# Performance work log

Measured on AMD Instinct MI355X. Metric: run time of the kernel, lower is better.

## Reference

```python
import jax, jax.numpy as jnp
import numpy as np

D = 256          # embed_dim
NH = 4           # num_heads
NE = 16          # num_hyperedges
TC = 512         # text_channels
WIN = 64         # window size
EPS = 1e-5


def setup_inputs() -> dict:
    key = jax.random.key(0)
    ks = jax.random.split(key, 20)
    s = 0.02
    return {
        "feature_map": jax.random.normal(ks[0], (8, 256, 64, 64), jnp.float32),
        "text_features": jax.random.normal(ks[1], (8, 64, TC), jnp.float32),
        # qkv_gen: Conv2d(256->256,1x1), GELU, Conv2d(256->768,3x3,pad1), GroupNorm(4,768)
        "conv1_w": jax.random.normal(ks[2], (D, 256, 1, 1), jnp.float32) * s,
        "conv1_b": jnp.zeros((D,), jnp.float32),
        "conv2_w": jax.random.normal(ks[3], (3 * D, D, 3, 3), jnp.float32) * s,
        "conv2_b": jnp.zeros((3 * D,), jnp.float32),
        "gn_w": jnp.ones((3 * D,), jnp.float32),
        "gn_b": jnp.zeros((3 * D,), jnp.float32),
        # shared nn.MultiheadAttention params
        "in_proj_w": jax.random.normal(ks[4], (3 * D, D), jnp.float32) * s,
        "in_proj_b": jnp.zeros((3 * D,), jnp.float32),
        "out_proj_w": jax.random.normal(ks[5], (D, D), jnp.float32) * s,
        "out_proj_b": jnp.zeros((D,), jnp.float32),
        # text_adapter Linear(512->256)
        "txt_w": jax.random.normal(ks[6], (D, TC), jnp.float32) * s,
        "txt_b": jnp.zeros((D,), jnp.float32),
        # edge_predictor: Linear(512->256), GELU, Linear(256->16)
        "ep1_w": jax.random.normal(ks[7], (D, 2 * D), jnp.float32) * s,
        "ep1_b": jnp.zeros((D,), jnp.float32),
        "ep2_w": jax.random.normal(ks[8], (NE, D), jnp.float32) * s,
        "ep2_b": jnp.zeros((NE,), jnp.float32),
    }


def _gelu(x):
    return jax.nn.gelu(x, approximate=False)  # torch default is exact erf GELU


def _conv(x, w, b, pad):
    y = jax.lax.conv_general_dilated(x, w, (1, 1), [(pad, pad), (pad, pad)],
                                     dimension_numbers=("NCHW", "OIHW", "NCHW"))
    return y + b[None, :, None, None]


def _group_norm(x, w, b, groups=4):
    B, C, H, W = x.shape
    xg = x.reshape(B, groups, C // groups, H, W)
    mu = xg.mean(axis=(2, 3, 4), keepdims=True)
    var = xg.var(axis=(2, 3, 4), keepdims=True)
    xg = (xg - mu) * jax.lax.rsqrt(var + EPS)
    return xg.reshape(B, C, H, W) * w[None, :, None, None] + b[None, :, None, None]


def _mha(q, k, v, in_w, in_b, out_w, out_b):
    # torch nn.MultiheadAttention (batch_first), same-dim q/k/v
    Wq, Wk, Wv = in_w[:D], in_w[D:2 * D], in_w[2 * D:]
    bq, bk, bv = in_b[:D], in_b[D:2 * D], in_b[2 * D:]
    dh = D // NH

    def split(x, W, bias):
        y = x @ W.T + bias                      # [B,L,D]
        Bv, L, _ = y.shape
        return y.reshape(Bv, L, NH, dh).transpose(0, 2, 1, 3)  # [B,H,L,dh]

    qh, kh, vh = split(q, Wq, bq), split(k, Wk, bk), split(v, Wv, bv)
    scores = jnp.einsum("bhqd,bhkd->bhqk", qh, kh) / jnp.sqrt(jnp.float32(dh))
    attn = jax.nn.softmax(scores, axis=-1)
    o = jnp.einsum("bhqk,bhkd->bhqd", attn, vh)
    Bv, _, Lq, _ = o.shape
    o = o.transpose(0, 2, 1, 3).reshape(Bv, Lq, D)
    return o @ out_w.T + out_b


def reference(feature_map, text_features, conv1_w, conv1_b, conv2_w, conv2_b,
              gn_w, gn_b, in_proj_w, in_proj_b, out_proj_w, out_proj_b,
              txt_w, txt_b, ep1_w, ep1_b, ep2_w, ep2_b):
    B, C, H, W = feature_map.shape
    N = H * W
    # qkv_gen
    x = _gelu(_conv(feature_map, conv1_w, conv1_b, 0))
    qkv = _group_norm(_conv(x, conv2_w, conv2_b, 1), gn_w, gn_b)
    q, k, v = jnp.split(qkv, 3, axis=1)                    # each [B,D,H,W]
    to_seq = lambda t: t.reshape(B, D, N).transpose(0, 2, 1)  # [B,N,D]
    q_seq, k_seq, v_seq = to_seq(q), to_seq(k), to_seq(v)

    # text_adapter: Linear then AdaptiveAvgPool1d(4) over sequence (L=64 -> 4 bins of 16)
    t = text_features @ txt_w.T + txt_b                    # [B,L,D]
    L = t.shape[1]
    text_feat = t.reshape(B, 4, L // 4, D).mean(axis=2)    # [B,4,D]

    # hierarchical attention
    nw = N // WIN
    q_win = q_seq.reshape(B * nw, WIN, D)
    k_win = k_seq.reshape(B * nw, WIN, D)
    v_win = v_seq.reshape(B * nw, WIN, D)
    local = _mha(q_win, k_win, v_win, in_proj_w, in_proj_b, out_proj_w, out_proj_b)
    local = local.reshape(B, nw, WIN, D)
    global_q = local.mean(axis=2)                          # [B,nw,D]
    glob = _mha(global_q, text_feat, text_feat, in_proj_w, in_proj_b, out_proj_w, out_proj_b)
    glob = jnp.broadcast_to(glob[:, :, None, :], (B, nw, WIN, D))

    combined = jnp.concatenate([local.reshape(B, N, D), glob.reshape(B, N, D)], axis=-1)
    h = _gelu(combined @ ep1_w.T + ep1_b)
    return jax.nn.sigmoid(h @ ep2_w.T + ep2_b)             # [B,N,16]
```

## Files before the change

kernel.cpp:

```cpp
#include <hip/hip_runtime.h>

#define DEV __device__ __forceinline__

typedef __attribute__((ext_vector_type(8))) short bfx8;
typedef __attribute__((ext_vector_type(4))) float fx4;

typedef __attribute__((address_space(3))) unsigned int as3_u32;
typedef const __attribute__((address_space(1))) unsigned int as1_u32c;

DEV void gl_lds16(const void* g, const void* l) {
  __builtin_amdgcn_global_load_lds((as1_u32c*)(unsigned long long)g,
                                   (as3_u32*)(unsigned long long)l, 16, 0, 0);
}

DEV short f2bf(float f) {
  unsigned u = __float_as_uint(f);
  u += 0x7fffu + ((u >> 16) & 1u);
  return (short)(u >> 16);
}
DEV float bf2f(short s) {
  return __uint_as_float(((unsigned)(unsigned short)s) << 16);
}
DEV float gelu_f(float x) { return 0.5f * x * (1.0f + erff(x * 0.70710678118654752f)); }

#define MFMA16(acc, a, b) (acc) = __builtin_amdgcn_mfma_f32_16x16x32_bf16((a), (b), (acc), 0, 0, 0)

struct CvtSeg { const float* src; short* dst; int n; };
struct CvtArgs { CvtSeg s[7]; };

__global__ __launch_bounds__(256) void cvt_multi(CvtArgs a) {
  CvtSeg s = a.s[blockIdx.y];
  int i = ((int)blockIdx.x * 256 + (int)threadIdx.x) * 8;
  if (i >= s.n) return;
  bfx8 o;
  #pragma unroll
  for (int j = 0; j < 8; ++j) o[j] = f2bf(s.src[i + j]);
  *(bfx8*)(s.dst + i) = o;
}

__global__ __launch_bounds__(256) void cvt_conv2w(const float* src, short* dst) {
  int oc = (int)blockIdx.x * 256 + (int)threadIdx.x;
  const float* s = src + (long)oc * 9;
  float t[9];
  #pragma unroll
  for (int j = 0; j < 9; ++j) t[j] = s[j];
  #pragma unroll
  for (int tap = 0; tap < 9; ++tap)
    dst[(long)tap * (768 * 256) + oc] = f2bf(t[tap]);
}

__global__ __launch_bounds__(256) void transpose_wo(const float* ow, short* WoT) {
  __shared__ float tile[64][65];
  int c0 = blockIdx.x * 64, d0 = blockIdx.y * 64;
  int tp = threadIdx.x & 63, tr = threadIdx.x >> 6;
  #pragma unroll
  for (int i = 0; i < 16; ++i) {
    int c = tr + i * 4;
    tile[c][tp] = ow[(long)(c0 + c) * 256 + d0 + tp];
  }
  __syncthreads();
  #pragma unroll
  for (int i = 0; i < 16; ++i) {
    int d = tr + i * 4;
    WoT[(long)(d0 + d) * 256 + c0 + tp] = f2bf(tile[tp][d]);
  }
}

__global__ __launch_bounds__(64) void ebc2(const float* e1w, const float* e1b, const float* ob, float* ebc) {
  int n = blockIdx.x, lane = threadIdx.x;
  float s = 0.0f;
  #pragma unroll
  for (int i = 0; i < 4; ++i) {
    int c = lane + 64 * i;
    s += ob[c] * e1w[(long)n * 512 + c];
  }
  #pragma unroll
  for (int off = 1; off < 64; off <<= 1) s += __shfl_xor(s, off);
  if (lane == 0) ebc[n] = e1b[n] + s;
}

DEV int axc(int p, int c) { return p * 260 + (c ^ (((p >> 2) & 7) << 2)); }

__global__ __launch_bounds__(256) void tc1(const float* fm, const short* W1bf,
                                           const float* b1, short* xP) {
  __shared__ float Af[64 * 260];
  const int lane = threadIdx.x & 63, wv = threadIdx.x >> 6;
  const int lg = lane >> 4, li = lane & 15;
  const int y = blockIdx.x & 63, b = blockIdx.x >> 6;
  const float* src = fm + (long)b * 256 * 4096 + y * 64;
  #pragma unroll
  for (int i = 0; i < 16; ++i) {
    int chunk = i * 256 + (int)threadIdx.x;
    int c = chunk >> 4;
    int q = chunk & 15;
    fx4 v = *(const fx4*)(src + (long)c * 4096 + q * 4);
    #pragma unroll
    for (int j = 0; j < 4; ++j) Af[axc(q * 4 + j, c)] = v[j];
  }
  __syncthreads();

  fx4 acc[4][4] = {};
  const short* Bb = W1bf + (long)(wv * 64 + li) * 256 + lg * 8;
  for (int c0 = 0; c0 < 256; c0 += 32) {
    bfx8 af[4], bfr[4];
    #pragma unroll
    for (int mi = 0; mi < 4; ++mi) {
      int p = mi * 16 + li;
      fx4 lo = *(const fx4*)(&Af[axc(p, c0 + lg * 8)]);
      fx4 hi = *(const fx4*)(&Af[axc(p, c0 + lg * 8 + 4)]);
      bfx8 t;
      t[0] = f2bf(lo[0]); t[1] = f2bf(lo[1]); t[2] = f2bf(lo[2]); t[3] = f2bf(lo[3]);
      t[4] = f2bf(hi[0]); t[5] = f2bf(hi[1]); t[6] = f2bf(hi[2]); t[7] = f2bf(hi[3]);
      af[mi] = t;
    }
    #pragma unroll
    for (int ni = 0; ni < 4; ++ni) bfr[ni] = *(const bfx8*)(Bb + ni * 16 * 256 + c0);
    #pragma unroll
    for (int mi = 0; mi < 4; ++mi)
      #pragma unroll
      for (int ni = 0; ni < 4; ++ni) MFMA16(acc[mi][ni], af[mi], bfr[ni]);
  }

  short* dstP = xP + ((long)b * 66 * 66 + (long)(y + 1) * 66 + 1) * 256;
  #pragma unroll
  for (int mi = 0; mi < 4; ++mi)
    #pragma unroll
    for (int ni = 0; ni < 4; ++ni) {
      int col = wv * 64 + ni * 16 + li;
      float bias = b1[col];
      #pragma unroll
      for (int r = 0; r < 4; ++r) {
        int x = mi * 16 + 4 * lg + r;
        dstP[(long)x * 256 + col] = f2bf(gelu_f(acc[mi][ni][r] + bias));
      }
    }
}

struct GemmP {
  const short* A; const short* B; void* O;
  const float* biasN; const float* biasM; const float* rowbias;
  long lda, ldb, ldo, sA, sB, sO;
  int M, N, K, outF32, act, padHW;
  int aShift;
  long sBN, sBM;
};

__global__ __launch_bounds__(256) void gemm128(GemmP g) {
  __shared__ short As[128 * 32];
  __shared__ short Bs[128 * 32];
  const int lane = threadIdx.x & 63, wv = threadIdx.x >> 6;
  const int wm = wv >> 1, wn = wv & 1;
  const int lg = lane >> 4, li = lane & 15;
  const int m0 = blockIdx.y * 128, n0 = blockIdx.x * 128, z = blockIdx.z;
  const short* A = g.A + (long)z * g.sA + (long)(n0 >> 8) * g.aShift;
  const short* B = g.B + (long)z * g.sB;
  const int srow = wv * 16 + (lane >> 2);
  const int scol = (lane & 3) * 8;
  const short* pA0 = A + (long)(m0 + srow) * g.lda + scol;
  const short* pA1 = A + (long)(m0 + 64 + srow) * g.lda + scol;
  const short* pB0 = B + (long)(n0 + srow) * g.ldb + scol;
  const short* pB1 = B + (long)(n0 + 64 + srow) * g.ldb + scol;
  short* ldsA = As + wv * 512;
  short* ldsB = Bs + wv * 512;
  const short* aRd = As + (wm * 64 + li) * 32 + lg * 8;
  const short* bRd = Bs + (wn * 64 + li) * 32 + lg * 8;

  fx4 acc[4][4] = {};
  for (int kc = 0; kc < g.K; kc += 32) {
    gl_lds16(pA0 + kc, ldsA);
    gl_lds16(pA1 + kc, ldsA + 2048);
    gl_lds16(pB0 + kc, ldsB);
    gl_lds16(pB1 + kc, ldsB + 2048);
    __syncthreads();
    bfx8 af[4], bf[4];
    #pragma unroll
    for (int mi = 0; mi < 4; ++mi) af[mi] = *(const bfx8*)(aRd + mi * 16 * 32);
    #pragma unroll
    for (int ni = 0; ni < 4; ++ni) bf[ni] = *(const bfx8*)(bRd + ni * 16 * 32);
    #pragma unroll
    for (int mi = 0; mi < 4; ++mi)
      #pragma unroll
      for (int ni = 0; ni < 4; ++ni)
        MFMA16(acc[mi][ni], af[mi], bf[ni]);
    __syncthreads();
  }

  #pragma unroll
  for (int mi = 0; mi < 4; ++mi)
    #pragma unroll
    for (int ni = 0; ni < 4; ++ni) {
      int col = n0 + wn * 64 + ni * 16 + li;
      int rowb = m0 + wm * 64 + mi * 16 + 4 * lg;
      float bn = g.biasN ? g.biasN[(long)z * g.sBN + col] : 0.0f;
      #pragma unroll
      for (int r = 0; r < 4; ++r) {
        int row = rowb + r;
        float v = acc[mi][ni][r] + bn;
        if (g.biasM) v += g.biasM[(long)z * g.sBM + row];
        if (g.rowbias) v += g.rowbias[(long)(row >> 6) * g.N + col];
        if (g.act == 1) v = gelu_f(v);
        long orow = row;
        if (g.padHW) orow = (long)((row >> 6) + 1) * 66 + (row & 63) + 1;
        long oidx = (long)z * g.sO + orow * g.ldo + col;
        if (g.outF32) ((float*)g.O)[oidx] = v;
        else ((short*)g.O)[oidx] = f2bf(v);
      }
    }
}

__global__ __launch_bounds__(256) void conv2g(const short* xP, const short* W2t,
                                              const float* b2, short* qkv, float* stats) {
  __shared__ short As[2 * 128 * 32];
  __shared__ short Bs[2 * 128 * 32];
  __shared__ float red[4][4];
  const int lane = threadIdx.x & 63, wv = threadIdx.x >> 6;
  const int wm = wv >> 1, wn = wv & 1;
  const int lg = lane >> 4, li = lane & 15;
  const int w = ((int)blockIdx.x & 7) * 192 + ((int)blockIdx.x >> 3);
  const int n0 = (w % 6) * 128;
  const int by = w / 6;
  const int b = by >> 5, ypair = by & 31;
  const short* xPb = xP + (long)b * 66 * 66 * 256;

  const int srow = wv * 16 + (lane >> 2);
  const int scol = (lane & 3) * 8;
  long baseA[2], baseB[2];
  #pragma unroll
  for (int j = 0; j < 2; ++j) {
    int r = j * 64 + srow;
    int yy = 2 * ypair + (r >> 6);
    int x = r & 63;
    baseA[j] = ((long)yy * 66 + x) * 256 + scol;
    baseB[j] = (long)(n0 + r) * 256 + scol;
  }
  short* ldsA = As + wv * 512;
  short* ldsB = Bs + wv * 512;
  const short* aRd = As + (wm * 64 + li) * 32 + lg * 8;
  const short* bRd = Bs + (wn * 64 + li) * 32 + lg * 8;

  fx4 acc[4][4] = {};
  for (int ks = 0; ks < 36; ++ks) {
    int tap = ks >> 2;
    int c0 = (ks & 3) * 64;
    int dy = tap / 3, dx = tap - dy * 3;
    long aoff = (long)(dy * 66 + dx) * 256 + c0;
    long boff = (long)tap * (768 * 256) + c0;
    gl_lds16(xPb + baseA[0] + aoff, ldsA);
    gl_lds16(xPb + baseA[1] + aoff, ldsA + 2048);
    gl_lds16(xPb + baseA[0] + aoff + 32, ldsA + 4096);
    gl_lds16(xPb + baseA[1] + aoff + 32, ldsA + 6144);
    gl_lds16(W2t + baseB[0] + boff, ldsB);
    gl_lds16(W2t + baseB[1] + boff, ldsB + 2048);
    gl_lds16(W2t + baseB[0] + boff + 32, ldsB + 4096);
    gl_lds16(W2t + baseB[1] + boff + 32, ldsB + 6144);
    __syncthreads();
    #pragma unroll
    for (int kk = 0; kk < 2; ++kk) {
      bfx8 af[4], bf[4];
      #pragma unroll
      for (int mi = 0; mi < 4; ++mi) af[mi] = *(const bfx8*)(aRd + kk * 4096 + mi * 16 * 32);
      #pragma unroll
      for (int ni = 0; ni < 4; ++ni) bf[ni] = *(const bfx8*)(bRd + kk * 4096 + ni * 16 * 32);
      #pragma unroll
      for (int mi = 0; mi < 4; ++mi)
        #pragma unroll
        for (int ni = 0; ni < 4; ++ni)
          MFMA16(acc[mi][ni], af[mi], bf[ni]);
    }
    __syncthreads();
  }

  const int g0 = n0 / 192;
  const int bnd = (g0 + 1) * 192;
  float sA = 0.0f, s2A = 0.0f, sB = 0.0f, s2B = 0.0f;
  const long prow0 = (long)b * 4096 + (long)ypair * 128 + wm * 64 + 4 * lg;
  #pragma unroll
  for (int ni = 0; ni < 4; ++ni) {
    int col = n0 + wn * 64 + ni * 16 + li;
    float bias = b2[col];
    bool inA = (col < bnd);
    #pragma unroll
    for (int mi = 0; mi < 4; ++mi) {
      long rb = prow0 + mi * 16;
      #pragma unroll
      for (int r = 0; r < 4; ++r) {
        float v = acc[mi][ni][r] + bias;
        if (inA) { sA += v; s2A += v * v; } else { sB += v; s2B += v * v; }
        qkv[(rb + r) * 768 + col] = f2bf(v);
      }
    }
  }
  #pragma unroll
  for (int off = 1; off < 64; off <<= 1) {
    sA += __shfl_xor(sA, off);  s2A += __shfl_xor(s2A, off);
    sB += __shfl_xor(sB, off);  s2B += __shfl_xor(s2B, off);
  }
  if (lane == 0) { red[wv][0] = sA; red[wv][1] = s2A; red[wv][2] = sB; red[wv][3] = s2B; }
  __syncthreads();
  if (threadIdx.x == 0) {
    float a1 = red[0][0] + red[1][0] + red[2][0] + red[3][0];
    float a2 = red[0][1] + red[1][1] + red[2][1] + red[3][1];
    atomicAdd(&stats[(b * 4 + g0) * 2], a1);
    atomicAdd(&stats[(b * 4 + g0) * 2 + 1], a2);
    if (bnd < n0 + 128) {
      float b1s = red[0][2] + red[1][2] + red[2][2] + red[3][2];
      float b2s = red[0][3] + red[1][3] + red[2][3] + red[3][3];
      atomicAdd(&stats[(b * 4 + g0 + 1) * 2], b1s);
      atomicAdd(&stats[(b * 4 + g0 + 1) * 2 + 1], b2s);
    }
  }
}

__global__ void gn_fin(const float* stats, float* mufs) {
  int i = threadIdx.x;
  if (i >= 32) return;
  float n = 192.0f * 4096.0f;
  float mu = stats[i * 2] / n;
  float var = stats[i * 2 + 1] / n - mu * mu;
  mufs[i * 2] = mu;
  mufs[i * 2 + 1] = rsqrtf(var + 1e-5f);
}

__global__ __launch_bounds__(256) void gn_fold(const float* mufs, const float* gnw, const float* gnb,
                                               const float* inw, const float* inb,
                                               short* Wf, float* bfold) {
  const int lane = threadIdx.x & 63, wv = threadIdx.x >> 6;
  const int row = blockIdx.x * 4 + wv;
  const int b = row / 768, j = row - b * 768;
  const int cb = (j >> 8) << 8;
  float part = 0.0f;
  #pragma unroll
  for (int i = 0; i < 4; ++i) {
    int c = lane + 64 * i;
    int cg = cb + c;
    int grp = cg / 192;
    float mu = mufs[(b * 4 + grp) * 2];
    float rs = mufs[(b * 4 + grp) * 2 + 1];
    float s = rs * gnw[cg];
    float t = gnb[cg] - mu * s;
    float wv_ = inw[(long)j * 256 + c];
    Wf[(long)row * 256 + c] = f2bf(wv_ * s);
    part += t * wv_;
  }
  #pragma unroll
  for (int off = 1; off < 64; off <<= 1) part += __shfl_xor(part, off);
  if (lane == 0) bfold[row] = inb[j] + part;
}

__global__ __launch_bounds__(256) void globk_txt(const short* Tbf, const short* Wtxt,
                                                 const short* Wqkv, const float* tb,
                                                 const float* inb, float* khv, float* vhv) {
  __shared__ float tmean_s[4][512];
  __shared__ float tfb_s[4][256];
  const int t = threadIdx.x;
  const int b = blockIdx.x;
  {
    int key = t >> 6, d0 = (t & 63) * 8;
    float s[8] = {};
    const short* src = Tbf + ((long)(b * 64 + key * 16)) * 512 + d0;
    for (int i = 0; i < 16; ++i) {
      bfx8 v = *(const bfx8*)(src + i * 512);
      #pragma unroll
      for (int j = 0; j < 8; ++j) s[j] += bf2f(v[j]);
    }
    #pragma unroll
    for (int j = 0; j < 8; ++j) tmean_s[key][d0 + j] = s[j] * (1.0f / 16.0f);
  }
  __syncthreads();
  {
    int n = t;
    float a0 = 0, a1 = 0, a2 = 0, a3 = 0;
    const short* wr = Wtxt + (long)n * 512;
    for (int d = 0; d < 512; d += 8) {
      bfx8 w = *(const bfx8*)(wr + d);
      #pragma unroll
      for (int j = 0; j < 8; ++j) {
        float wf = bf2f(w[j]);
        a0 += tmean_s[0][d + j] * wf;
        a1 += tmean_s[1][d + j] * wf;
        a2 += tmean_s[2][d + j] * wf;
        a3 += tmean_s[3][d + j] * wf;
      }
    }
    float bias = tb[n];
    tfb_s[0][n] = a0 + bias; tfb_s[1][n] = a1 + bias;
    tfb_s[2][n] = a2 + bias; tfb_s[3][n] = a3 + bias;
  }
  __syncthreads();
  {
    int n = t;
    const short* wk = Wqkv + (long)(256 + n) * 256;
    const short* wvp = Wqkv + (long)(512 + n) * 256;
    float k0=0,k1=0,k2=0,k3=0,v0=0,v1=0,v2=0,v3=0;
    for (int d = 0; d < 256; d += 8) {
      bfx8 wkv = *(const bfx8*)(wk + d);
      bfx8 wvv = *(const bfx8*)(wvp + d);
      #pragma unroll
      for (int j = 0; j < 8; ++j) {
        float f0 = tfb_s[0][d+j], f1 = tfb_s[1][d+j], f2 = tfb_s[2][d+j], f3 = tfb_s[3][d+j];
        float kw = bf2f(wkv[j]), vw = bf2f(wvv[j]);
        k0 += f0*kw; k1 += f1*kw; k2 += f2*kw; k3 += f3*kw;
        v0 += f0*vw; v1 += f1*vw; v2 += f2*vw; v3 += f3*vw;
      }
    }
    float bk = inb[256+n], bv = inb[512+n];
    khv[(b*4+0)*256+n]=k0+bk; khv[(b*4+1)*256+n]=k1+bk;
    khv[(b*4+2)*256+n]=k2+bk; khv[(b*4+3)*256+n]=k3+bk;
    vhv[(b*4+0)*256+n]=v0+bv; vhv[(b*4+1)*256+n]=v1+bv;
    vhv[(b*4+2)*256+n]=v2+bv; vhv[(b*4+3)*256+n]=v3+bv;
  }
}

__global__ __launch_bounds__(256) void attn_mega(
    const short* qk, const short* vhT, const float* khv, const float* vhv,
    const short* Wo, const short* Wqkv, const short* Wep1, const short* Wcomb, const short* Wep2,
    const float* ob, const float* inb, const float* ebc, const float* e2b,
    float* out) {
  __shared__ short Pl[4 * 64 * 72];
  __shared__ float vecA[256], vecB[256], vecG[256];
  __shared__ float scb[16], pb[16];
  const int t = threadIdx.x;
  const int lane = t & 63, h = t >> 6;
  const int lg = lane >> 4, li = lane & 15;
  const int bw = blockIdx.x;
  const int b = bw >> 6, wY = bw & 63;
  const long p0 = (long)bw * 64;

  bfx8 qf[4][2], kf[4][2];
  #pragma unroll
  for (int mi = 0; mi < 4; ++mi)
    #pragma unroll
    for (int ks = 0; ks < 2; ++ks) {
      qf[mi][ks] = *(const bfx8*)(qk + (p0 + 16 * mi + li) * 512 + h * 64 + 32 * ks + 8 * lg);
      kf[mi][ks] = *(const bfx8*)(qk + (p0 + 16 * mi + li) * 512 + 256 + h * 64 + 32 * ks + 8 * lg);
    }
  fx4 s[4][4] = {};
  #pragma unroll
  for (int mi = 0; mi < 4; ++mi)
    #pragma unroll
    for (int ni = 0; ni < 4; ++ni) {
      MFMA16(s[mi][ni], qf[mi][0], kf[ni][0]);
      MFMA16(s[mi][ni], qf[mi][1], kf[ni][1]);
    }
  #pragma unroll
  for (int mi = 0; mi < 4; ++mi)
    #pragma unroll
    for (int ni = 0; ni < 4; ++ni) s[mi][ni] *= 0.125f;

  #pragma unroll
  for (int mi = 0; mi < 4; ++mi)
    #pragma unroll
    for (int r = 0; r < 4; ++r) {
      float mx = fmaxf(fmaxf(s[mi][0][r], s[mi][1][r]), fmaxf(s[mi][2][r], s[mi][3][r]));
      for (int off = 1; off < 16; off <<= 1) mx = fmaxf(mx, __shfl_xor(mx, off));
      float e[4];
      float sum = 0.0f;
      #pragma unroll
      for (int ni = 0; ni < 4; ++ni) { e[ni] = expf(s[mi][ni][r] - mx); sum += e[ni]; }
      for (int off = 1; off < 16; off <<= 1) sum += __shfl_xor(sum, off);
      float inv = 1.0f / sum;
      int row = h * 64 + 16 * mi + 4 * lg + r;
      #pragma unroll
      for (int ni = 0; ni < 4; ++ni) Pl[row * 72 + 16 * ni + li] = f2bf(e[ni] * inv);
    }
  __syncthreads();

  fx4 o[4][4] = {};
  #pragma unroll
  for (int ks = 0; ks < 2; ++ks) {
    bfx8 pf[4], vf[4];
    #pragma unroll
    for (int mi = 0; mi < 4; ++mi)
      pf[mi] = *(const bfx8*)(&Pl[(h * 64 + 16 * mi + li) * 72 + 32 * ks + 8 * lg]);
    #pragma unroll
    for (int ni = 0; ni < 4; ++ni)
      vf[ni] = *(const bfx8*)(vhT + ((long)(b * 256 + h * 64 + 16 * ni + li)) * 4096 + wY * 64 + 32 * ks + 8 * lg);
    #pragma unroll
    for (int mi = 0; mi < 4; ++mi)
      #pragma unroll
      for (int ni = 0; ni < 4; ++ni) MFMA16(o[mi][ni], pf[mi], vf[ni]);
  }

  #pragma unroll
  for (int ni = 0; ni < 4; ++ni) {
    float s2 = 0.0f;
    #pragma unroll
    for (int mi = 0; mi < 4; ++mi)
      #pragma unroll
      for (int r = 0; r < 4; ++r) s2 += o[mi][ni][r];
    s2 += __shfl_xor(s2, 16);
    s2 += __shfl_xor(s2, 32);
    if (lg == 0) vecA[h * 64 + 16 * ni + li] = s2 * (1.0f / 64.0f);
  }
  __syncthreads();

  short* obuf = Pl;
  #pragma unroll
  for (int mi = 0; mi < 4; ++mi)
    #pragma unroll
    for (int ni = 0; ni < 4; ++ni)
      #pragma unroll
      for (int r = 0; r < 4; ++r)
        obuf[(16 * mi + 4 * lg + r) * 264 + h * 64 + 16 * ni + li] = f2bf(o[mi][ni][r]);

  {
    float sum = 0.0f;
    const short* wr = Wo + (long)t * 256;
    for (int d = 0; d < 256; d += 8) {
      bfx8 w8 = *(const bfx8*)(wr + d);
      #pragma unroll
      for (int j = 0; j < 8; ++j) sum += vecA[d + j] * bf2f(w8[j]);
    }
    vecB[t] = sum + ob[t];
  }
  __syncthreads();
  {
    float sum = 0.0f;
    const short* wr = Wqkv + (long)t * 256;
    for (int d = 0; d < 256; d += 8) {
      bfx8 w8 = *(const bfx8*)(wr + d);
      #pragma unroll
      for (int j = 0; j < 8; ++j) sum += vecB[d + j] * bf2f(w8[j]);
    }
    vecG[t] = sum + inb[t];
  }
  __syncthreads();
  if (t < 16) {
    int key = t & 3, hh = t >> 2;
    float sum = 0.0f;
    const float* kr = khv + (long)(b * 4 + key) * 256 + hh * 64;
    for (int d = 0; d < 64; ++d) sum += vecG[hh * 64 + d] * kr[d];
    scb[hh * 4 + key] = sum * 0.125f;
  }
  __syncthreads();
  if (t < 4) {
    float s0 = scb[t*4], s1 = scb[t*4+1], s2 = scb[t*4+2], s3 = scb[t*4+3];
    float mx = fmaxf(fmaxf(s0, s1), fmaxf(s2, s3));
    float e0 = expf(s0-mx), e1 = expf(s1-mx), e2 = expf(s2-mx), e3 = expf(s3-mx);
    float inv = 1.0f / (e0 + e1 + e2 + e3);
    pb[t*4] = e0*inv; pb[t*4+1] = e1*inv; pb[t*4+2] = e2*inv; pb[t*4+3] = e3*inv;
  }
  __syncthreads();
  {
    int hh = t >> 6;
    long base = (long)(b * 4) * 256 + t;
    vecB[t] = pb[hh*4]   * vhv[base] +
              pb[hh*4+1] * vhv[base + 256] +
              pb[hh*4+2] * vhv[base + 512] +
              pb[hh*4+3] * vhv[base + 768];
  }
  __syncthreads();
  {
    float sum = 0.0f;
    const short* wr = Wo + (long)t * 256;
    for (int d = 0; d < 256; d += 8) {
      bfx8 w8 = *(const bfx8*)(wr + d);
      #pragma unroll
      for (int j = 0; j < 8; ++j) sum += vecB[d + j] * bf2f(w8[j]);
    }
    vecA[t] = sum + ob[t];
  }
  __syncthreads();
  {
    float sum = 0.0f;
    const short* wr = Wep1 + (long)t * 512 + 256;
    for (int d = 0; d < 256; d += 8) {
      bfx8 w8 = *(const bfx8*)(wr + d);
      #pragma unroll
      for (int j = 0; j < 8; ++j) sum += vecA[d + j] * bf2f(w8[j]);
    }
    vecG[t] = sum + ebc[t];
  }
  __syncthreads();

  fx4 hacc[4][4] = {};
  const short* bR2 = Wcomb + (long)(h * 64 + li) * 256 + lg * 8;
  for (int kc = 0; kc < 256; kc += 32) {
    bfx8 af[4], bf[4];
    #pragma unroll
    for (int mi = 0; mi < 4; ++mi)
      af[mi] = *(const bfx8*)(obuf + (mi * 16 + li) * 264 + kc + lg * 8);
    #pragma unroll
    for (int ni = 0; ni < 4; ++ni) bf[ni] = *(const bfx8*)(bR2 + (long)ni * 16 * 256 + kc);
    #pragma unroll
    for (int mi = 0; mi < 4; ++mi)
      #pragma unroll
      for (int ni = 0; ni < 4; ++ni) MFMA16(hacc[mi][ni], af[mi], bf[ni]);
  }
  __syncthreads();
  #pragma unroll
  for (int mi = 0; mi < 4; ++mi)
    #pragma unroll
    for (int ni = 0; ni < 4; ++ni) {
      int col = h * 64 + ni * 16 + li;
      #pragma unroll
      for (int r = 0; r < 4; ++r) {
        int row = mi * 16 + 4 * lg + r;
        obuf[row * 264 + col] = f2bf(gelu_f(hacc[mi][ni][r] + vecG[col]));
      }
    }
  __syncthreads();

  {
    int row = t >> 2, eg = (t & 3) * 4;
    const short* hr = obuf + row * 264;
    float a0 = e2b[eg], a1 = e2b[eg+1], a2 = e2b[eg+2], a3 = e2b[eg+3];
    const short* w0 = Wep2 + (long)eg * 256;
    for (int k = 0; k < 256; k += 8) {
      bfx8 hv = *(const bfx8*)(hr + k);
      bfx8 wv0 = *(const bfx8*)(w0 + k);
      bfx8 wv1 = *(const bfx8*)(w0 + 256 + k);
      bfx8 wv2 = *(const bfx8*)(w0 + 512 + k);
      bfx8 wv3 = *(const bfx8*)(w0 + 768 + k);
      #pragma unroll
      for (int j = 0; j < 8; ++j) {
        float hf = bf2f(hv[j]);
        a0 += hf * bf2f(wv0[j]);
        a1 += hf * bf2f(wv1[j]);
        a2 += hf * bf2f(wv2[j]);
        a3 += hf * bf2f(wv3[j]);
      }
    }
    float* orow = out + (p0 + row) * 16 + eg;
    orow[0] = 1.0f / (1.0f + expf(-a0));
    orow[1] = 1.0f / (1.0f + expf(-a1));
    orow[2] = 1.0f / (1.0f + expf(-a2));
    orow[3] = 1.0f / (1.0f + expf(-a3));
  }
}

extern "C" void kernel_launch(void* const* d_in, const int* in_sizes, int n_in,
                              void* d_out, int out_size, void* d_ws, size_t ws_size,
                              hipStream_t stream) {
  (void)in_sizes; (void)n_in; (void)out_size; (void)ws_size;
  const float* fm  = (const float*)d_in[0];
  const float* txt = (const float*)d_in[1];
  const float* w1  = (const float*)d_in[2];
  const float* b1  = (const float*)d_in[3];
  const float* w2  = (const float*)d_in[4];
  const float* b2  = (const float*)d_in[5];
  const float* gnw = (const float*)d_in[6];
  const float* gnb = (const float*)d_in[7];
  const float* inw = (const float*)d_in[8];
  const float* inb = (const float*)d_in[9];
  const float* ow  = (const float*)d_in[10];
  const float* ob  = (const float*)d_in[11];
  const float* tw  = (const float*)d_in[12];
  const float* tb  = (const float*)d_in[13];
  const float* e1w = (const float*)d_in[14];
  const float* e1b = (const float*)d_in[15];
  const float* e2w = (const float*)d_in[16];
  const float* e2b = (const float*)d_in[17];
  float* out = (float*)d_out;

  char* base = (char*)d_ws;
  size_t off = 0;
  auto alloc = [&](size_t bytes) -> char* {
    char* r = base + off;
    off = (off + bytes + 255) & ~(size_t)255;
    return r;
  };
  short* W1bf = (short*)alloc(256 * 256 * 2);
  short* W2t  = (short*)alloc((size_t)9 * 768 * 256 * 2);
  short* Wqkv = (short*)alloc(768 * 256 * 2);
  short* Wo   = (short*)alloc(256 * 256 * 2);
  short* WoT  = (short*)alloc(256 * 256 * 2);
  short* Wcomb= (short*)alloc(256 * 256 * 2);
  float* ebc  = (float*)alloc(256 * 4);
  short* Wtxt = (short*)alloc(256 * 512 * 2);
  short* Wep1 = (short*)alloc(256 * 512 * 2);
  short* Wep2 = (short*)alloc(16 * 256 * 2);
  short* Tbf  = (short*)alloc((size_t)8 * 64 * 512 * 2);
  short* xP   = (short*)alloc((size_t)8 * 66 * 66 * 256 * 2);
  short* qkv  = (short*)alloc((size_t)8 * 4096 * 768 * 2);
  float* stats= (float*)alloc(64 * 4);
  float* mufs = (float*)alloc(64 * 4);
  short* Wf   = (short*)alloc((size_t)8 * 768 * 256 * 2);
  float* bfold= (float*)alloc((size_t)8 * 768 * 4);
  short* qk   = (short*)alloc((size_t)32768 * 512 * 2);
  short* vhT  = (short*)alloc((size_t)8 * 4096 * 256 * 2);
  float* khv  = (float*)alloc(8 * 4 * 256 * 4);
  float* vhv  = (float*)alloc(8 * 4 * 256 * 4);

  hipMemsetAsync(stats, 0, 64 * 4, stream);
  hipMemsetAsync(xP, 0, (size_t)8 * 66 * 66 * 256 * 2, stream);

  CvtArgs ca;
  ca.s[0] = {w1,  W1bf, 256 * 256};
  ca.s[1] = {inw, Wqkv, 768 * 256};
  ca.s[2] = {ow,  Wo,   256 * 256};
  ca.s[3] = {tw,  Wtxt, 256 * 512};
  ca.s[4] = {e1w, Wep1, 256 * 512};
  ca.s[5] = {e2w, Wep2, 16 * 256};
  ca.s[6] = {txt, Tbf,  8 * 64 * 512};
  cvt_multi<<<dim3(128, 7), 256, 0, stream>>>(ca);
  cvt_conv2w<<<768, 256, 0, stream>>>(w2, W2t);
  transpose_wo<<<dim3(4, 4), 256, 0, stream>>>(ow, WoT);
  ebc2<<<256, 64, 0, stream>>>(e1w, e1b, ob, ebc);
  globk_txt<<<8, 256, 0, stream>>>(Tbf, Wtxt, Wqkv, tb, inb, khv, vhv);

  {
    GemmP g{};
    g.A = Wep1; g.lda = 512; g.B = WoT; g.ldb = 256;
    g.O = Wcomb; g.ldo = 256;
    g.M = 256; g.N = 256; g.K = 256;
    gemm128<<<dim3(2, 2, 1), 256, 0, stream>>>(g);
  }

  tc1<<<512, 256, 0, stream>>>(fm, W1bf, b1, xP);

  conv2g<<<1536, 256, 0, stream>>>(xP, W2t, b2, qkv, stats);
  gn_fin<<<1, 32, 0, stream>>>(stats, mufs);
  gn_fold<<<1536, 256, 0, stream>>>(mufs, gnw, gnb, inw, inb, Wf, bfold);

  {
    GemmP g{};
    g.A = qkv; g.lda = 768; g.sA = 4096L * 768;
    g.B = Wf; g.ldb = 256; g.sB = 768L * 256;
    g.O = qk; g.ldo = 512; g.sO = 4096L * 512;
    g.biasN = bfold; g.sBN = 768;
    g.aShift = 256;
    g.M = 4096; g.N = 512; g.K = 256;
    gemm128<<<dim3(4, 32, 8), 256, 0, stream>>>(g);
  }
  {
    GemmP g{};
    g.A = Wf + 512 * 256; g.lda = 256; g.sA = 768L * 256;
    g.B = qkv + 512; g.ldb = 768; g.sB = 4096L * 768;
    g.O = vhT; g.ldo = 4096; g.sO = 256L * 4096;
    g.biasM = bfold + 512; g.sBM = 768;
    g.M = 256; g.N = 4096; g.K = 256;
    gemm128<<<dim3(32, 2, 8), 256, 0, stream>>>(g);
  }

  attn_mega<<<512, 256, 0, stream>>>(qk, vhT, khv, vhv,
                                     Wo, Wqkv, Wep1, Wcomb, Wep2,
                                     ob, inb, ebc, e2b, out);
}
```

Baseline: 382.8 us.

## Zero conv halos in-kernel, fuse small prep kernels, merge projection GEMM launches

The full-buffer memset of the padded conv input is removed; tc1 now writes zeros only into the halo rows and columns it owns. The transpose-plus-GEMM that builds Wcomb becomes one small kernel that transposes Wo into LDS. gn_fin is folded into gn_fold, and the Q/K and V projection GEMMs run as a single launch with a swizzled block mapping. conv2g is split into four launches of 384 blocks each. The aim is less memory traffic and fewer tiny launches, at the cost of extra per-launch overhead from the conv split.

Result: slower. 445.1 us (+16.3%).

```diff
diff --git a/kernel.cpp b/kernel.cpp
--- a/kernel.cpp
+++ b/kernel.cpp
@@ -49,23 +49,6 @@
     dst[(long)tap * (768 * 256) + oc] = f2bf(t[tap]);
 }
 
-__global__ __launch_bounds__(256) void transpose_wo(const float* ow, short* WoT) {
-  __shared__ float tile[64][65];
-  int c0 = blockIdx.x * 64, d0 = blockIdx.y * 64;
-  int tp = threadIdx.x & 63, tr = threadIdx.x >> 6;
-  #pragma unroll
-  for (int i = 0; i < 16; ++i) {
-    int c = tr + i * 4;
-    tile[c][tp] = ow[(long)(c0 + c) * 256 + d0 + tp];
-  }
-  __syncthreads();
-  #pragma unroll
-  for (int i = 0; i < 16; ++i) {
-    int d = tr + i * 4;
-    WoT[(long)(d0 + d) * 256 + c0 + tp] = f2bf(tile[tp][d]);
-  }
-}
-
 __global__ __launch_bounds__(64) void ebc2(const float* e1w, const float* e1b, const float* ob, float* ebc) {
   int n = blockIdx.x, lane = threadIdx.x;
   float s = 0.0f;
@@ -77,6 +60,34 @@
   #pragma unroll
   for (int off = 1; off < 64; off <<= 1) s += __shfl_xor(s, off);
   if (lane == 0) ebc[n] = e1b[n] + s;
+}
+
+__global__ __launch_bounds__(256) void wcombk(const float* ow, const short* Wep1, short* Wcomb) {
+  __shared__ short Bt[64 * 264];
+  const int t = threadIdx.x;
+  const int lane = t & 63, w = t >> 6;
+  const int lg = lane >> 4, li = lane & 15;
+  const int m0 = blockIdx.y * 64, n0 = blockIdx.x * 64;
+  for (int idx = t; idx < 64 * 256; idx += 256) {
+    int c = idx >> 6, d = idx & 63;
+    Bt[d * 264 + c] = f2bf(ow[(long)c * 256 + n0 + d]);
+  }
+  __syncthreads();
+  fx4 acc[4] = {};
+  const short* aR = Wep1 + (long)(m0 + w * 16 + li) * 512 + lg * 8;
+  for (int kc = 0; kc < 256; kc += 32) {
+    bfx8 a = *(const bfx8*)(aR + kc);
+    #pragma unroll
+    for (int ni = 0; ni < 4; ++ni) {
+      bfx8 bv = *(const bfx8*)(&Bt[(ni * 16 + li) * 264 + kc + lg * 8]);
+      MFMA16(acc[ni], a, bv);
+    }
+  }
+  #pragma unroll
+  for (int ni = 0; ni < 4; ++ni)
+    #pragma unroll
+    for (int r = 0; r < 4; ++r)
+      Wcomb[(long)(m0 + w * 16 + 4 * lg + r) * 256 + n0 + ni * 16 + li] = f2bf(acc[ni][r]);
 }
 
 DEV int axc(int p, int c) { return p * 260 + (c ^ (((p >> 2) & 7) << 2)); }
@@ -87,10 +98,27 @@
   const int lane = threadIdx.x & 63, wv = threadIdx.x >> 6;
   const int lg = lane >> 4, li = lane & 15;
   const int y = blockIdx.x & 63, b = blockIdx.x >> 6;
+  const int t = threadIdx.x;
+  short* dstP = xP + ((long)b * 66 * 66 + (long)(y + 1) * 66 + 1) * 256;
+  const bfx8 z8 = {0, 0, 0, 0, 0, 0, 0, 0};
+
+  if (t < 64) {
+    if (t < 32) *(bfx8*)(dstP - 256 + t * 8) = z8;
+    else        *(bfx8*)(dstP + 64 * 256 + (t - 32) * 8) = z8;
+  }
+  if (y == 0) {
+    short* top = xP + (long)b * 66 * 66 * 256;
+    for (int i = t; i < 2112; i += 256) *(bfx8*)(top + i * 8) = z8;
+  }
+  if (y == 63) {
+    short* bot = xP + ((long)b * 66 * 66 + 65 * 66) * 256;
+    for (int i = t; i < 2112; i += 256) *(bfx8*)(bot + i * 8) = z8;
+  }
+
   const float* src = fm + (long)b * 256 * 4096 + y * 64;
   #pragma unroll
   for (int i = 0; i < 16; ++i) {
-    int chunk = i * 256 + (int)threadIdx.x;
+    int chunk = i * 256 + t;
     int c = chunk >> 4;
     int q = chunk & 15;
     fx4 v = *(const fx4*)(src + (long)c * 4096 + q * 4);
@@ -108,10 +136,10 @@
       int p = mi * 16 + li;
       fx4 lo = *(const fx4*)(&Af[axc(p, c0 + lg * 8)]);
       fx4 hi = *(const fx4*)(&Af[axc(p, c0 + lg * 8 + 4)]);
-      bfx8 t;
-      t[0] = f2bf(lo[0]); t[1] = f2bf(lo[1]); t[2] = f2bf(lo[2]); t[3] = f2bf(lo[3]);
-      t[4] = f2bf(hi[0]); t[5] = f2bf(hi[1]); t[6] = f2bf(hi[2]); t[7] = f2bf(hi[3]);
-      af[mi] = t;
+      bfx8 tt;
+      tt[0] = f2bf(lo[0]); tt[1] = f2bf(lo[1]); tt[2] = f2bf(lo[2]); tt[3] = f2bf(lo[3]);
+      tt[4] = f2bf(hi[0]); tt[5] = f2bf(hi[1]); tt[6] = f2bf(hi[2]); tt[7] = f2bf(hi[3]);
+      af[mi] = tt;
     }
     #pragma unroll
     for (int ni = 0; ni < 4; ++ni) bfr[ni] = *(const bfx8*)(Bb + ni * 16 * 256 + c0);
@@ -121,7 +149,6 @@
       for (int ni = 0; ni < 4; ++ni) MFMA16(acc[mi][ni], af[mi], bfr[ni]);
   }
 
-  short* dstP = xP + ((long)b * 66 * 66 + (long)(y + 1) * 66 + 1) * 256;
   #pragma unroll
   for (int mi = 0; mi < 4; ++mi)
     #pragma unroll
@@ -145,13 +172,13 @@
   long sBN, sBM;
 };
 
-__global__ __launch_bounds__(256) void gemm128(GemmP g) {
+DEV void gemm_body(const GemmP& g, int bx, int by, int bz) {
   __shared__ short As[128 * 32];
   __shared__ short Bs[128 * 32];
   const int lane = threadIdx.x & 63, wv = threadIdx.x >> 6;
   const int wm = wv >> 1, wn = wv & 1;
   const int lg = lane >> 4, li = lane & 15;
-  const int m0 = blockIdx.y * 128, n0 = blockIdx.x * 128, z = blockIdx.z;
+  const int m0 = by * 128, n0 = bx * 128, z = bz;
   const short* A = g.A + (long)z * g.sA + (long)(n0 >> 8) * g.aShift;
   const short* B = g.B + (long)z * g.sB;
   const int srow = wv * 16 + (lane >> 2);
@@ -197,26 +224,36 @@
         int row = rowb + r;
         float v = acc[mi][ni][r] + bn;
         if (g.biasM) v += g.biasM[(long)z * g.sBM + row];
-        if (g.rowbias) v += g.rowbias[(long)(row >> 6) * g.N + col];
         if (g.act == 1) v = gelu_f(v);
-        long orow = row;
-        if (g.padHW) orow = (long)((row >> 6) + 1) * 66 + (row & 63) + 1;
-        long oidx = (long)z * g.sO + orow * g.ldo + col;
+        long oidx = (long)z * g.sO + (long)row * g.ldo + col;
         if (g.outF32) ((float*)g.O)[oidx] = v;
         else ((short*)g.O)[oidx] = f2bf(v);
       }
     }
 }
 
+__global__ __launch_bounds__(256) void projk(GemmP gq, GemmP gv) {
+  int bid = (int)blockIdx.x;
+  int id = (bid & 7) * 192 + (bid >> 3);
+  if (id < 1024) {
+    int z = id >> 7, r = id & 127;
+    gemm_body(gq, r & 3, r >> 2, z);
+  } else {
+    int j = id - 1024;
+    int z = j >> 6, r = j & 63;
+    gemm_body(gv, r & 31, r >> 5, z);
+  }
+}
+
 __global__ __launch_bounds__(256) void conv2g(const short* xP, const short* W2t,
-                                              const float* b2, short* qkv, float* stats) {
+                                              const float* b2, short* qkv, float* stats, int wbase) {
   __shared__ short As[2 * 128 * 32];
   __shared__ short Bs[2 * 128 * 32];
   __shared__ float red[4][4];
   const int lane = threadIdx.x & 63, wv = threadIdx.x >> 6;
   const int wm = wv >> 1, wn = wv & 1;
   const int lg = lane >> 4, li = lane & 15;
-  const int w = ((int)blockIdx.x & 7) * 192 + ((int)blockIdx.x >> 3);
+  const int w = wbase + (((int)blockIdx.x & 7) * 48 + ((int)blockIdx.x >> 3));
   const int n0 = (w % 6) * 128;
   const int by = w / 6;
   const int b = by >> 5, ypair = by & 31;
@@ -311,31 +348,25 @@
   }
 }
 
-__global__ void gn_fin(const float* stats, float* mufs) {
-  int i = threadIdx.x;
-  if (i >= 32) return;
-  float n = 192.0f * 4096.0f;
-  float mu = stats[i * 2] / n;
-  float var = stats[i * 2 + 1] / n - mu * mu;
-  mufs[i * 2] = mu;
-  mufs[i * 2 + 1] = rsqrtf(var + 1e-5f);
-}
-
-__global__ __launch_bounds__(256) void gn_fold(const float* mufs, const float* gnw, const float* gnb,
+__global__ __launch_bounds__(256) void gn_fold(const float* stats, const float* gnw, const float* gnb,
                                                const float* inw, const float* inb,
                                                short* Wf, float* bfold) {
   const int lane = threadIdx.x & 63, wv = threadIdx.x >> 6;
   const int row = blockIdx.x * 4 + wv;
   const int b = row / 768, j = row - b * 768;
   const int cb = (j >> 8) << 8;
+  const float nrm = 1.0f / (192.0f * 4096.0f);
   float part = 0.0f;
   #pragma unroll
   for (int i = 0; i < 4; ++i) {
     int c = lane + 64 * i;
     int cg = cb + c;
     int grp = cg / 192;
-    float mu = mufs[(b * 4 + grp) * 2];
-    float rs = mufs[(b * 4 + grp) * 2 + 1];
+    float s1 = stats[(b * 4 + grp) * 2];
+    float s2 = stats[(b * 4 + grp) * 2 + 1];
+    float mu = s1 * nrm;
+    float var = s2 * nrm - mu * mu;
+    float rs = rsqrtf(var + 1e-5f);
     float s = rs * gnw[cg];
     float t = gnb[cg] - mu * s;
     float wv_ = inw[(long)j * 256 + c];
@@ -664,7 +695,6 @@
   short* W2t  = (short*)alloc((size_t)9 * 768 * 256 * 2);
   short* Wqkv = (short*)alloc(768 * 256 * 2);
   short* Wo   = (short*)alloc(256 * 256 * 2);
-  short* WoT  = (short*)alloc(256 * 256 * 2);
   short* Wcomb= (short*)alloc(256 * 256 * 2);
   float* ebc  = (float*)alloc(256 * 4);
   short* Wtxt = (short*)alloc(256 * 512 * 2);
@@ -674,7 +704,6 @@
   short* xP   = (short*)alloc((size_t)8 * 66 * 66 * 256 * 2);
   short* qkv  = (short*)alloc((size_t)8 * 4096 * 768 * 2);
   float* stats= (float*)alloc(64 * 4);
-  float* mufs = (float*)alloc(64 * 4);
   short* Wf   = (short*)alloc((size_t)8 * 768 * 256 * 2);
   float* bfold= (float*)alloc((size_t)8 * 768 * 4);
   short* qk   = (short*)alloc((size_t)32768 * 512 * 2);
@@ -683,7 +712,6 @@
   float* vhv  = (float*)alloc(8 * 4 * 256 * 4);
 
   hipMemsetAsync(stats, 0, 64 * 4, stream);
-  hipMemsetAsync(xP, 0, (size_t)8 * 66 * 66 * 256 * 2, stream);
 
   CvtArgs ca;
   ca.s[0] = {w1,  W1bf, 256 * 256};
@@ -695,42 +723,34 @@
   ca.s[6] = {txt, Tbf,  8 * 64 * 512};
   cvt_multi<<<dim3(128, 7), 256, 0, stream>>>(ca);
   cvt_conv2w<<<768, 256, 0, stream>>>(w2, W2t);
-  transpose_wo<<<dim3(4, 4), 256, 0, stream>>>(ow, WoT);
   ebc2<<<256, 64, 0, stream>>>(e1w, e1b, ob, ebc);
   globk_txt<<<8, 256, 0, stream>>>(Tbf, Wtxt, Wqkv, tb, inb, khv, vhv);
-
-  {
-    GemmP g{};
-    g.A = Wep1; g.lda = 512; g.B = WoT; g.ldb = 256;
-    g.O = Wcomb; g.ldo = 256;
-    g.M = 256; g.N = 256; g.K = 256;
-    gemm128<<<dim3(2, 2, 1), 256, 0, stream>>>(g);
-  }
+  wcombk<<<dim3(4, 4), 256, 0, stream>>>(ow, Wep1, Wcomb);
 
   tc1<<<512, 256, 0, stream>>>(fm, W1bf, b1, xP);
 
-  conv2g<<<1536, 256, 0, stream>>>(xP, W2t, b2, qkv, stats);
-  gn_fin<<<1, 32, 0, stream>>>(stats, mufs);
-  gn_fold<<<1536, 256, 0, stream>>>(mufs, gnw, gnb, inw, inb, Wf, bfold);
-
-  {
-    GemmP g{};
-    g.A = qkv; g.lda = 768; g.sA = 4096L * 768;
-    g.B = Wf; g.ldb = 256; g.sB = 768L * 256;
-    g.O = qk; g.ldo = 512; g.sO = 4096L * 512;
-    g.biasN = bfold; g.sBN = 768;
-    g.aShift = 256;
-    g.M = 4096; g.N = 512; g.K = 256;
-    gemm128<<<dim3(4, 32, 8), 256, 0, stream>>>(g);
-  }
-  {
-    GemmP g{};
-    g.A = Wf + 512 * 256; g.lda = 256; g.sA = 768L * 256;
-    g.B = qkv + 512; g.ldb = 768; g.sB = 4096L * 768;
-    g.O = vhT; g.ldo = 4096; g.sO = 256L * 4096;
-    g.biasM = bfold + 512; g.sBM = 768;
-    g.M = 256; g.N = 4096; g.K = 256;
-    gemm128<<<dim3(32, 2, 8), 256, 0, stream>>>(g);
+  conv2g<<<384, 256, 0, stream>>>(xP, W2t, b2, qkv, stats, 0);
+  conv2g<<<384, 256, 0, stream>>>(xP, W2t, b2, qkv, stats, 384);
+  conv2g<<<384, 256, 0, stream>>>(xP, W2t, b2, qkv, stats, 768);
+  conv2g<<<384, 256, 0, stream>>>(xP, W2t, b2, qkv, stats, 1152);
+
+  gn_fold<<<1536, 256, 0, stream>>>(stats, gnw, gnb, inw, inb, Wf, bfold);
+
+  {
+    GemmP gq{};
+    gq.A = qkv; gq.lda = 768; gq.sA = 4096L * 768;
+    gq.B = Wf; gq.ldb = 256; gq.sB = 768L * 256;
+    gq.O = qk; gq.ldo = 512; gq.sO = 4096L * 512;
+    gq.biasN = bfold; gq.sBN = 768;
+    gq.aShift = 256;
+    gq.M = 4096; gq.N = 512; gq.K = 256;
+    GemmP gv{};
+    gv.A = Wf + 512 * 256; gv.lda = 256; gv.sA = 768L * 256;
+    gv.B = qkv + 512; gv.ldb = 768; gv.sB = 4096L * 768;
+    gv.O = vhT; gv.ldo = 4096; gv.sO = 256L * 4096;
+    gv.biasM = bfold + 512; gv.sBM = 768;
+    gv.M = 256; gv.N = 4096; gv.K = 256;
+    projk<<<1536, 256, 0, stream>>>(gq, gv);
   }
 
   attn_mega<<<512, 256, 0, stream>>>(qk, vhT, khv, vhv,
```
